# Kernel optimization log

Hardware: AMD Instinct MI355X
Metric: run time of the kernel (lower is better)

Reference implementation:

```python
import jax, jax.numpy as jnp
import numpy as np

B, S, D = 2, 2048, 768
E, F = 8, 3072  # num_experts, d_ff


def setup_inputs() -> dict:
    key = jax.random.key(0)
    k1, k2, k3, k4 = jax.random.split(key, 4)
    hidden_states = jax.random.normal(k1, (B, S, D), dtype=jnp.float32)
    w_router = jax.random.normal(k2, (D, E), dtype=jnp.float32) * (D ** -0.5)
    w1 = jax.random.normal(k3, (E, D, F), dtype=jnp.float32) * (D ** -0.5)
    w2 = jax.random.normal(k4, (E, F, D), dtype=jnp.float32) * (F ** -0.5)
    return {"hidden_states": hidden_states, "w_router": w_router, "w1": w1, "w2": w2}


def reference(hidden_states, w_router, w1, w2):
    # Router: top-1 (switch) routing.
    router_logits = jnp.einsum("bsd,de->bse", hidden_states, w_router)
    probs = jax.nn.softmax(router_logits, axis=-1)
    expert_index = jnp.argmax(probs, axis=-1)                      # [B,S] int
    router_mask = jax.nn.one_hot(expert_index, E, dtype=hidden_states.dtype)  # [B,S,E]
    router_probs = jnp.max(probs, axis=-1, keepdims=True)          # [B,S,1]

    # Expert FFN dispatch/combine (world_size=1 -> all_to_all is identity):
    # each token is processed by its assigned expert's relu-MLP.
    h1 = jax.nn.relu(jnp.einsum("bsd,edf->ebsf", hidden_states, w1))  # [E,B,S,F]
    h2 = jnp.einsum("ebsf,efd->ebsd", h1, w2)                          # [E,B,S,D]
    expert_out = jnp.einsum("ebsd,bse->bsd", h2, router_mask)          # combine

    out = router_probs * expert_out
    return out, router_logits, expert_index
```

## Files before the change

kernel.cpp:

```cpp
#include <hip/hip_runtime.h>
#include <hip/hip_bf16.h>

#define B_ 2
#define S_ 2048
#define D_ 768
#define E_ 8
#define F_ 3072
#define NT (B_*S_)
#define BM 128
#define MAXTILES 40

typedef __attribute__((ext_vector_type(8))) short bf16x8;
typedef __attribute__((ext_vector_type(4))) float f32x4;
typedef __attribute__((ext_vector_type(8))) unsigned short u16x8;

__device__ __forceinline__ unsigned short f2bf(float f){
  __hip_bfloat16 h = __float2bfloat16(f);
  return *reinterpret_cast<unsigned short*>(&h);
}

__device__ __forceinline__ void gll16(const void* g, void* l){
  __builtin_amdgcn_global_load_lds((const __attribute__((address_space(1))) unsigned int*)g,
                                   (__attribute__((address_space(3))) unsigned int*)l,
                                   16, 0, 0);
}

__global__ __launch_bounds__(256) void router_kernel(
    const float* __restrict__ x, const float* __restrict__ wr,
    float* __restrict__ logits_out, float* __restrict__ idx_out,
    float* __restrict__ probs, int* __restrict__ counts,
    int* __restrict__ bucket, unsigned short* __restrict__ xbf)
{
  const int wave = threadIdx.x >> 6, lane = threadIdx.x & 63;
  const int token = blockIdx.x * 4 + wave;
  const float* xp = x + (size_t)token * D_;

  float acc[E_] = {0.f,0.f,0.f,0.f,0.f,0.f,0.f,0.f};
  float xv[12];
  #pragma unroll
  for (int i = 0; i < 12; ++i){
    const int d = lane + i*64;
    const float v = xp[d];
    xv[i] = v;
    const float4 w0 = *(const float4*)(wr + d*8);
    const float4 w1 = *(const float4*)(wr + d*8 + 4);
    acc[0] += v*w0.x; acc[1] += v*w0.y; acc[2] += v*w0.z; acc[3] += v*w0.w;
    acc[4] += v*w1.x; acc[5] += v*w1.y; acc[6] += v*w1.z; acc[7] += v*w1.w;
  }
  #pragma unroll
  for (int j = 0; j < E_; ++j){
    float a = acc[j];
    for (int off = 32; off > 0; off >>= 1) a += __shfl_xor(a, off);
    acc[j] = a;
  }
  #pragma unroll
  for (int i = 0; i < 12; ++i){
    const int d = lane + i*64;
    xbf[(size_t)token * D_ + d] = f2bf(xv[i]);
  }
  if (lane == 0){
    float m = acc[0];
    #pragma unroll
    for (int j = 1; j < E_; ++j) m = fmaxf(m, acc[j]);
    float p[E_]; float s = 0.f;
    #pragma unroll
    for (int j = 0; j < E_; ++j){ p[j] = expf(acc[j] - m); s += p[j]; }
    const float inv = 1.0f / s;
    int best = 0; float bp = p[0]*inv;
    #pragma unroll
    for (int j = 1; j < E_; ++j){ const float pj = p[j]*inv; if (pj > bp){ bp = pj; best = j; } }
    float* lo = logits_out + (size_t)token * E_;
    #pragma unroll
    for (int j = 0; j < E_; ++j) lo[j] = acc[j];
    idx_out[token] = (float)best;
    probs[token] = bp;
    const int pos = atomicAdd(&counts[best], 1);
    bucket[best * NT + pos] = token;
  }
}

__global__ void build_tiles(const int* __restrict__ counts, int* __restrict__ meta)
{
  if (threadIdx.x == 0 && blockIdx.x == 0){
    int off = 0, n = 0;
    for (int e = 0; e < E_; ++e){
      const int c = counts[e];
      meta[1+e] = off;
      const int t = (c + BM - 1) / BM;
      for (int m = 0; m < t; ++m){ meta[16 + n] = (e << 16) | m; ++n; }
      off += c;
    }
    meta[0] = n;
  }
}

__global__ __launch_bounds__(256) void transpose_cvt(
    const float* __restrict__ in, unsigned short* __restrict__ outp, int R, int C)
{
  __shared__ float tile[64][65];
  const int e = blockIdx.z;
  const int r0 = blockIdx.y << 6, c0 = blockIdx.x << 6;
  const float* src = in + (size_t)e * R * C;
  unsigned short* dst = outp + (size_t)e * R * C;
  const int tid = threadIdx.x;
  {
    const int lr = tid >> 4, lc = (tid & 15) << 2;
    #pragma unroll
    for (int rr = 0; rr < 4; ++rr){
      const int row = (rr << 4) + lr;
      const float4 v = *(const float4*)(src + (size_t)(r0 + row) * C + c0 + lc);
      tile[row][lc+0] = v.x; tile[row][lc+1] = v.y;
      tile[row][lc+2] = v.z; tile[row][lc+3] = v.w;
    }
  }
  __syncthreads();
  {
    const int wrr = tid >> 3, wcc = (tid & 7) << 3;
    #pragma unroll
    for (int it = 0; it < 2; ++it){
      const int crow = (it << 5) + wrr;
      u16x8 o;
      #pragma unroll
      for (int j = 0; j < 8; ++j) o[j] = f2bf(tile[wcc + j][crow]);
      *(u16x8*)(dst + (size_t)(c0 + crow) * R + r0 + wcc) = o;
    }
  }
}

template<int K, int NCOLS, bool RELU>
__global__ __launch_bounds__(256) void gemm2ph(
    const unsigned short* __restrict__ Ab, const unsigned short* __restrict__ Bt,
    const int* __restrict__ counts, const int* __restrict__ bucket,
    const int* __restrict__ meta, const float* __restrict__ probs,
    unsigned short* __restrict__ h1out, float* __restrict__ fout)
{
  __shared__ unsigned short As[2][BM*64];
  __shared__ unsigned short Bs[2][128*64];
  if ((int)blockIdx.y >= meta[0]) return;
  const int em = meta[16 + blockIdx.y];
  const int e = em >> 16, mt = em & 0xffff;
  const int cnt = counts[e], off_e = meta[1+e];
  const int fbase = blockIdx.x << 7;
  const int tid = threadIdx.x, wave = tid >> 6, lane = tid & 63;
  const int* bkt = bucket + e * NT;
  const int rbase = mt * BM;

  const int rsub = lane >> 3;
  const int swzb = ((lane & 7) ^ rsub) << 4;
  const int cm1 = cnt - 1;
  const char* Asrc[4]; const char* Bsrc[4];
  #pragma unroll
  for (int c = 0; c < 4; ++c){
    const int cw = (c << 2) + wave;
    const int row = (cw << 3) + rsub;
    int gr = rbase + row; if (gr > cm1) gr = cm1;
    const size_t arow = RELU ? (size_t)bkt[gr] : (size_t)(off_e + gr);
    Asrc[c] = (const char*)(Ab + arow * K) + swzb;
    Bsrc[c] = (const char*)(Bt + ((size_t)e * NCOLS + fbase + row) * K) + swzb;
  }

  f32x4 acc[4][4] = {};
  const int wr = (wave >> 1) << 6;
  const int wc = (wave & 1) << 6;
  const int lo16 = lane & 15, hi = lane >> 4;
  constexpr int KT = K / 64;

  auto STAGE = [&](int buf, int kt){
    const int kb = kt << 7;
    #pragma unroll
    for (int c = 0; c < 4; ++c){
      const int cw = (c << 2) + wave;
      gll16(Asrc[c] + kb, (char*)&As[buf][0] + (cw << 10));
      gll16(Bsrc[c] + kb, (char*)&Bs[buf][0] + (cw << 10));
    }
  };
  auto COMPUTE = [&](int buf){
    const char* AsB = (const char*)&As[buf][0];
    const char* BsB = (const char*)&Bs[buf][0];
    #pragma unroll
    for (int kf = 0; kf < 2; ++kf){
      const int ko = (kf << 6) + (hi << 4);
      bf16x8 af[4], bv[4];
      #pragma unroll
      for (int mf = 0; mf < 4; ++mf){
        const int row = wr + (mf << 4) + lo16;
        af[mf] = *(const bf16x8*)(AsB + row * 128 + (ko ^ ((row & 7) << 4)));
      }
      #pragma unroll
      for (int nf = 0; nf < 4; ++nf){
        const int col = wc + (nf << 4) + lo16;
        bv[nf] = *(const bf16x8*)(BsB + col * 128 + (ko ^ ((col & 7) << 4)));
      }
      #pragma unroll
      for (int mf = 0; mf < 4; ++mf)
        #pragma unroll
        for (int nf = 0; nf < 4; ++nf)
          acc[mf][nf] = __builtin_amdgcn_mfma_f32_16x16x32_bf16(af[mf], bv[nf], acc[mf][nf], 0, 0, 0);
    }
  };

  STAGE(0, 0);
  __syncthreads();
  int cur = 0;
  for (int kt = 0; kt < KT - 1; ++kt){
    STAGE(cur ^ 1, kt + 1);
    COMPUTE(cur);
    __syncthreads();
    cur ^= 1;
  }
  COMPUTE(cur);

  const int rem = cnt - rbase;
  #pragma unroll
  for (int mf = 0; mf < 4; ++mf){
    #pragma unroll
    for (int j = 0; j < 4; ++j){
      const int r = wr + (mf << 4) + (hi << 2) + j;
      if (r < rem){
        if constexpr (RELU){
          const size_t crow = (size_t)(off_e + rbase + r);
          #pragma unroll
          for (int nf = 0; nf < 4; ++nf){
            float v = acc[mf][nf][j];
            v = v > 0.f ? v : 0.f;
            h1out[crow * NCOLS + fbase + wc + (nf << 4) + lo16] = f2bf(v);
          }
        } else {
          const int tok = bkt[rbase + r];
          const float p = probs[tok];
          #pragma unroll
          for (int nf = 0; nf < 4; ++nf)
            fout[(size_t)tok * NCOLS + fbase + wc + (nf << 4) + lo16] = p * acc[mf][nf][j];
        }
      }
    }
  }
}

extern "C" void kernel_launch(void* const* d_in, const int* in_sizes, int n_in,
                              void* d_out, int out_size, void* d_ws, size_t ws_size,
                              hipStream_t stream)
{
  const float* x  = (const float*)d_in[0];
  const float* wr = (const float*)d_in[1];
  const float* w1 = (const float*)d_in[2];
  const float* w2 = (const float*)d_in[3];
  float* out = (float*)d_out;

  constexpr size_t OUT_L = (size_t)NT * D_;
  constexpr size_t OUT_I = OUT_L + (size_t)NT * E_;

  char* ws = (char*)d_ws;
  int*            counts = (int*)ws;
  int*            meta   = (int*)(ws + 256);
  float*          probs  = (float*)(ws + 1024);
  int*            bucket = (int*)(ws + (32u << 10));
  unsigned short* xbf    = (unsigned short*)(ws + (256u << 10));
  unsigned short* w1t    = (unsigned short*)(ws + (8ull  << 20));
  unsigned short* w2t    = (unsigned short*)(ws + (48ull << 20));
  unsigned short* h1c    = (unsigned short*)(ws + (88ull << 20));

  hipMemsetAsync(counts, 0, E_ * sizeof(int), stream);

  router_kernel<<<dim3(NT/4), dim3(256), 0, stream>>>(
      x, wr, out + OUT_L, out + OUT_I, probs, counts, bucket, xbf);

  build_tiles<<<dim3(1), dim3(64), 0, stream>>>(counts, meta);

  transpose_cvt<<<dim3(F_/64, D_/64, E_), dim3(256), 0, stream>>>(w1, w1t, D_, F_);
  transpose_cvt<<<dim3(D_/64, F_/64, E_), dim3(256), 0, stream>>>(w2, w2t, F_, D_);

  gemm2ph<D_, F_, true><<<dim3(F_/128, MAXTILES), dim3(256), 0, stream>>>(
      xbf, w1t, counts, bucket, meta, nullptr, h1c, nullptr);

  gemm2ph<F_, D_, false><<<dim3(D_/128, MAXTILES), dim3(256), 0, stream>>>(
      h1c, w2t, counts, bucket, meta, probs, nullptr, out);
}
```

Measured before the change: 339.8 us.

## Gather tokens per expert, enlarge GEMM tiles, add split-K with atomic combine

The router now processes 16 tokens per wave and uses wave-ballot aggregated atomics to fill the per-expert buckets. A new gather_cvt kernel writes the tokens contiguously, grouped by expert, as bf16, so the first GEMM no longer does indirect row loads. Both expert GEMMs move to 256x128x128 tiles on 512-thread blocks, with an XCD-aware workgroup remap. The second GEMM is split in two along K and combines its halves with float atomicAdd into a zeroed output. In exchange, LDS double-buffering is dropped (load, sync, compute), and the change adds an extra memset, an extra kernel and atomic traffic.

New measurement: 362.5 us. 6.7% more time.

```diff
diff --git a/kernel.cpp b/kernel.cpp
--- a/kernel.cpp
+++ b/kernel.cpp
@@ -7,8 +7,10 @@
 #define E_ 8
 #define F_ 3072
 #define NT (B_*S_)
-#define BM 128
-#define MAXTILES 40
+#define BM 256
+#define BN 128
+#define BK 128
+#define MAXT 24
 
 typedef __attribute__((ext_vector_type(8))) short bf16x8;
 typedef __attribute__((ext_vector_type(4))) float f32x4;
@@ -28,54 +30,66 @@
 __global__ __launch_bounds__(256) void router_kernel(
     const float* __restrict__ x, const float* __restrict__ wr,
     float* __restrict__ logits_out, float* __restrict__ idx_out,
-    float* __restrict__ probs, int* __restrict__ counts,
-    int* __restrict__ bucket, unsigned short* __restrict__ xbf)
-{
+    float* __restrict__ probs, int* __restrict__ counts, int* __restrict__ bucket)
+{
+  __shared__ int sbest[64];
   const int wave = threadIdx.x >> 6, lane = threadIdx.x & 63;
-  const int token = blockIdx.x * 4 + wave;
-  const float* xp = x + (size_t)token * D_;
-
-  float acc[E_] = {0.f,0.f,0.f,0.f,0.f,0.f,0.f,0.f};
-  float xv[12];
-  #pragma unroll
-  for (int i = 0; i < 12; ++i){
-    const int d = lane + i*64;
-    const float v = xp[d];
-    xv[i] = v;
-    const float4 w0 = *(const float4*)(wr + d*8);
-    const float4 w1 = *(const float4*)(wr + d*8 + 4);
-    acc[0] += v*w0.x; acc[1] += v*w0.y; acc[2] += v*w0.z; acc[3] += v*w0.w;
-    acc[4] += v*w1.x; acc[5] += v*w1.y; acc[6] += v*w1.z; acc[7] += v*w1.w;
-  }
-  #pragma unroll
-  for (int j = 0; j < E_; ++j){
-    float a = acc[j];
-    for (int off = 32; off > 0; off >>= 1) a += __shfl_xor(a, off);
-    acc[j] = a;
-  }
-  #pragma unroll
-  for (int i = 0; i < 12; ++i){
-    const int d = lane + i*64;
-    xbf[(size_t)token * D_ + d] = f2bf(xv[i]);
-  }
-  if (lane == 0){
-    float m = acc[0];
-    #pragma unroll
-    for (int j = 1; j < E_; ++j) m = fmaxf(m, acc[j]);
-    float p[E_]; float s = 0.f;
-    #pragma unroll
-    for (int j = 0; j < E_; ++j){ p[j] = expf(acc[j] - m); s += p[j]; }
-    const float inv = 1.0f / s;
-    int best = 0; float bp = p[0]*inv;
-    #pragma unroll
-    for (int j = 1; j < E_; ++j){ const float pj = p[j]*inv; if (pj > bp){ bp = pj; best = j; } }
-    float* lo = logits_out + (size_t)token * E_;
-    #pragma unroll
-    for (int j = 0; j < E_; ++j) lo[j] = acc[j];
-    idx_out[token] = (float)best;
-    probs[token] = bp;
-    const int pos = atomicAdd(&counts[best], 1);
-    bucket[best * NT + pos] = token;
+  const int tbase = blockIdx.x * 64 + wave * 16;
+
+  for (int it = 0; it < 16; ++it){
+    const int token = tbase + it;
+    const float* xp = x + (size_t)token * D_;
+    float acc[E_] = {0.f,0.f,0.f,0.f,0.f,0.f,0.f,0.f};
+    #pragma unroll
+    for (int i = 0; i < 12; ++i){
+      const int d = lane + i*64;
+      const float v = xp[d];
+      const float4 w0 = *(const float4*)(wr + d*8);
+      const float4 w1v = *(const float4*)(wr + d*8 + 4);
+      acc[0] += v*w0.x; acc[1] += v*w0.y; acc[2] += v*w0.z; acc[3] += v*w0.w;
+      acc[4] += v*w1v.x; acc[5] += v*w1v.y; acc[6] += v*w1v.z; acc[7] += v*w1v.w;
+    }
+    #pragma unroll
+    for (int j = 0; j < E_; ++j){
+      float a = acc[j];
+      for (int off = 32; off > 0; off >>= 1) a += __shfl_xor(a, off);
+      acc[j] = a;
+    }
+    if (lane == 0){
+      float m = acc[0];
+      #pragma unroll
+      for (int j = 1; j < E_; ++j) m = fmaxf(m, acc[j]);
+      float p[E_]; float s = 0.f;
+      #pragma unroll
+      for (int j = 0; j < E_; ++j){ p[j] = expf(acc[j] - m); s += p[j]; }
+      const float inv = 1.0f / s;
+      int best = 0; float bp = p[0]*inv;
+      #pragma unroll
+      for (int j = 1; j < E_; ++j){ const float pj = p[j]*inv; if (pj > bp){ bp = pj; best = j; } }
+      float* lo = logits_out + (size_t)token * E_;
+      #pragma unroll
+      for (int j = 0; j < E_; ++j) lo[j] = acc[j];
+      idx_out[token] = (float)best;
+      probs[token] = bp;
+      sbest[wave*16 + it] = best;
+    }
+  }
+  __syncthreads();
+  if (threadIdx.x < 64){
+    const int l = threadIdx.x;
+    const int b = sbest[l];
+    unsigned long long m = 0;
+    #pragma unroll
+    for (int e2 = 0; e2 < E_; ++e2){
+      const unsigned long long me = __ballot(b == e2);
+      if (b == e2) m = me;
+    }
+    const int rank = __popcll(m & ((1ull << l) - 1ull));
+    const int leader = __ffsll((long long)m) - 1;
+    int baseval = 0;
+    if (l == leader) baseval = atomicAdd(&counts[b], __popcll(m));
+    baseval = __shfl(baseval, leader);
+    bucket[b * NT + baseval + rank] = blockIdx.x * 64 + l;
   }
 }
 
@@ -87,10 +101,31 @@
       const int c = counts[e];
       meta[1+e] = off;
       const int t = (c + BM - 1) / BM;
-      for (int m = 0; m < t; ++m){ meta[16 + n] = (e << 16) | m; ++n; }
+      for (int mtt = 0; mtt < t; ++mtt){ meta[16 + n] = (e << 16) | mtt; ++n; }
       off += c;
     }
     meta[0] = n;
+  }
+}
+
+__global__ __launch_bounds__(256) void gather_cvt(
+    const float* __restrict__ x, const int* __restrict__ bucket,
+    const int* __restrict__ meta, unsigned short* __restrict__ Ac)
+{
+  const int wave = threadIdx.x >> 6, lane = threadIdx.x & 63;
+  const int i = blockIdx.x * 4 + wave;
+  int e = 0;
+  #pragma unroll
+  for (int k = 1; k < E_; ++k) if (meta[1+k] <= i) e = k;
+  const int tok = bucket[e * NT + (i - meta[1+e])];
+  const float* src = x + (size_t)tok * D_;
+  unsigned short* dst = Ac + (size_t)i * D_;
+  #pragma unroll
+  for (int p = 0; p < 3; ++p){
+    const float4 v = *(const float4*)(src + p*256 + lane*4);
+    ushort4 o;
+    o.x = f2bf(v.x); o.y = f2bf(v.y); o.z = f2bf(v.z); o.w = f2bf(v.w);
+    *(ushort4*)(dst + p*256 + lane*4) = o;
   }
 }
 
@@ -127,69 +162,81 @@
   }
 }
 
-template<int K, int NCOLS, bool RELU>
-__global__ __launch_bounds__(256) void gemm2ph(
-    const unsigned short* __restrict__ Ab, const unsigned short* __restrict__ Bt,
+template<int KC, int KTOT, int NCOLS, bool RELU, int NSPLIT>
+__global__ __launch_bounds__(512) void gemm_g(
+    const unsigned short* __restrict__ Ac, const unsigned short* __restrict__ Bt,
     const int* __restrict__ counts, const int* __restrict__ bucket,
     const int* __restrict__ meta, const float* __restrict__ probs,
     unsigned short* __restrict__ h1out, float* __restrict__ fout)
 {
-  __shared__ unsigned short As[2][BM*64];
-  __shared__ unsigned short Bs[2][128*64];
-  if ((int)blockIdx.y >= meta[0]) return;
-  const int em = meta[16 + blockIdx.y];
+  __shared__ unsigned short As[BM*BK];
+  __shared__ unsigned short Bs[BN*BK];
+
+  const int nwg = gridDim.x * gridDim.y * gridDim.z;
+  const int orig = ((int)blockIdx.z * gridDim.y + blockIdx.y) * gridDim.x + blockIdx.x;
+  const int q = nwg >> 3, r = nwg & 7;
+  const int xcd = orig & 7, jj = orig >> 3;
+  const int wgid = (xcd < r ? xcd*(q+1) : r*(q+1) + (xcd - r)*q) + jj;
+  constexpr int NTC = NCOLS / BN;
+  const int nt = wgid % NTC;
+  const int rest = wgid / NTC;
+  const int ks = (NSPLIT > 1) ? (rest % NSPLIT) : 0;
+  const int tile = (NSPLIT > 1) ? (rest / NSPLIT) : rest;
+  if (tile >= meta[0]) return;
+
+  const int em = meta[16 + tile];
   const int e = em >> 16, mt = em & 0xffff;
   const int cnt = counts[e], off_e = meta[1+e];
-  const int fbase = blockIdx.x << 7;
+  const int rbase = mt * BM;
+  const int fbase = nt * BN;
   const int tid = threadIdx.x, wave = tid >> 6, lane = tid & 63;
-  const int* bkt = bucket + e * NT;
-  const int rbase = mt * BM;
-
-  const int rsub = lane >> 3;
-  const int swzb = ((lane & 7) ^ rsub) << 4;
+  const int rsub = lane >> 4;
+  const int c16 = lane & 15;
   const int cm1 = cnt - 1;
-  const char* Asrc[4]; const char* Bsrc[4];
+
+  const char* Asrc[8]; const char* Bsrc[4];
+  #pragma unroll
+  for (int c = 0; c < 8; ++c){
+    const int row = ((wave + (c << 3)) << 2) + rsub;
+    int gr = rbase + row; if (gr > cm1) gr = cm1;
+    Asrc[c] = (const char*)(Ac + (size_t)(off_e + gr) * KTOT + ks * KC)
+              + ((c16 ^ (row & 15)) << 4);
+  }
   #pragma unroll
   for (int c = 0; c < 4; ++c){
-    const int cw = (c << 2) + wave;
-    const int row = (cw << 3) + rsub;
-    int gr = rbase + row; if (gr > cm1) gr = cm1;
-    const size_t arow = RELU ? (size_t)bkt[gr] : (size_t)(off_e + gr);
-    Asrc[c] = (const char*)(Ab + arow * K) + swzb;
-    Bsrc[c] = (const char*)(Bt + ((size_t)e * NCOLS + fbase + row) * K) + swzb;
-  }
-
-  f32x4 acc[4][4] = {};
+    const int row = ((wave + (c << 3)) << 2) + rsub;
+    Bsrc[c] = (const char*)(Bt + ((size_t)e * NCOLS + fbase + row) * KTOT + ks * KC)
+              + ((c16 ^ (row & 15)) << 4);
+  }
+
   const int wr = (wave >> 1) << 6;
   const int wc = (wave & 1) << 6;
   const int lo16 = lane & 15, hi = lane >> 4;
-  constexpr int KT = K / 64;
-
-  auto STAGE = [&](int buf, int kt){
-    const int kb = kt << 7;
-    #pragma unroll
-    for (int c = 0; c < 4; ++c){
-      const int cw = (c << 2) + wave;
-      gll16(Asrc[c] + kb, (char*)&As[buf][0] + (cw << 10));
-      gll16(Bsrc[c] + kb, (char*)&Bs[buf][0] + (cw << 10));
-    }
-  };
-  auto COMPUTE = [&](int buf){
-    const char* AsB = (const char*)&As[buf][0];
-    const char* BsB = (const char*)&Bs[buf][0];
-    #pragma unroll
-    for (int kf = 0; kf < 2; ++kf){
+  f32x4 acc[4][4] = {};
+  constexpr int NKT = KC / BK;
+
+  for (int kt = 0; kt < NKT; ++kt){
+    const int kb = kt * (BK * 2);
+    #pragma unroll
+    for (int c = 0; c < 8; ++c)
+      gll16(Asrc[c] + kb, (char*)As + ((wave + (c << 3)) << 10));
+    #pragma unroll
+    for (int c = 0; c < 4; ++c)
+      gll16(Bsrc[c] + kb, (char*)Bs + ((wave + (c << 3)) << 10));
+    __syncthreads();
+    #pragma unroll
+    for (int kf = 0; kf < 4; ++kf){
       const int ko = (kf << 6) + (hi << 4);
       bf16x8 af[4], bv[4];
       #pragma unroll
       for (int mf = 0; mf < 4; ++mf){
         const int row = wr + (mf << 4) + lo16;
-        af[mf] = *(const bf16x8*)(AsB + row * 128 + (ko ^ ((row & 7) << 4)));
+        af[mf] = *(const bf16x8*)((const char*)As + row * 256 + (ko ^ ((row & 15) << 4)));
       }
       #pragma unroll
       for (int nf = 0; nf < 4; ++nf){
         const int col = wc + (nf << 4) + lo16;
-        bv[nf] = *(const bf16x8*)(BsB + col * 128 + (ko ^ ((col & 7) << 4)));
+        bv[nf] = *(const bf16x8*)((const char*)Bs + col * 256 + (ko ^ ((col & 15) << 4)));
       }
       #pragma unroll
       for (int mf = 0; mf < 4; ++mf)
@@ -197,28 +244,18 @@
         for (int nf = 0; nf < 4; ++nf)
           acc[mf][nf] = __builtin_amdgcn_mfma_f32_16x16x32_bf16(af[mf], bv[nf], acc[mf][nf], 0, 0, 0);
     }
-  };
-
-  STAGE(0, 0);
-  __syncthreads();
-  int cur = 0;
-  for (int kt = 0; kt < KT - 1; ++kt){
-    STAGE(cur ^ 1, kt + 1);
-    COMPUTE(cur);
     __syncthreads();
-    cur ^= 1;
-  }
-  COMPUTE(cur);
+  }
 
   const int rem = cnt - rbase;
   #pragma unroll
   for (int mf = 0; mf < 4; ++mf){
     #pragma unroll
     for (int j = 0; j < 4; ++j){
-      const int r = wr + (mf << 4) + (hi << 2) + j;
-      if (r < rem){
+      const int rr2 = wr + (mf << 4) + (hi << 2) + j;
+      if (rr2 < rem){
         if constexpr (RELU){
-          const size_t crow = (size_t)(off_e + rbase + r);
+          const size_t crow = (size_t)(off_e + rbase + rr2);
           #pragma unroll
           for (int nf = 0; nf < 4; ++nf){
             float v = acc[mf][nf][j];
@@ -226,11 +263,12 @@
             h1out[crow * NCOLS + fbase + wc + (nf << 4) + lo16] = f2bf(v);
           }
         } else {
-          const int tok = bkt[rbase + r];
+          const int tok = bucket[e * NT + rbase + rr2];
           const float p = probs[tok];
           #pragma unroll
           for (int nf = 0; nf < 4; ++nf)
-            fout[(size_t)tok * NCOLS + fbase + wc + (nf << 4) + lo16] = p * acc[mf][nf][j];
+            atomicAdd(&fout[(size_t)tok * NCOLS + fbase + wc + (nf << 4) + lo16],
+                      p * acc[mf][nf][j]);
         }
       }
     }
@@ -255,24 +293,27 @@
   int*            meta   = (int*)(ws + 256);
   float*          probs  = (float*)(ws + 1024);
   int*            bucket = (int*)(ws + (32u << 10));
-  unsigned short* xbf    = (unsigned short*)(ws + (256u << 10));
+  unsigned short* Ac     = (unsigned short*)(ws + (256u << 10));
   unsigned short* w1t    = (unsigned short*)(ws + (8ull  << 20));
   unsigned short* w2t    = (unsigned short*)(ws + (48ull << 20));
   unsigned short* h1c    = (unsigned short*)(ws + (88ull << 20));
 
   hipMemsetAsync(counts, 0, E_ * sizeof(int), stream);
-
-  router_kernel<<<dim3(NT/4), dim3(256), 0, stream>>>(
-      x, wr, out + OUT_L, out + OUT_I, probs, counts, bucket, xbf);
+  hipMemsetAsync(out, 0, OUT_L * sizeof(float), stream);
+
+  router_kernel<<<dim3(NT/64), dim3(256), 0, stream>>>(
+      x, wr, out + OUT_L, out + OUT_I, probs, counts, bucket);
 
   build_tiles<<<dim3(1), dim3(64), 0, stream>>>(counts, meta);
+
+  gather_cvt<<<dim3(NT/4), dim3(256), 0, stream>>>(x, bucket, meta, Ac);
 
   transpose_cvt<<<dim3(F_/64, D_/64, E_), dim3(256), 0, stream>>>(w1, w1t, D_, F_);
   transpose_cvt<<<dim3(D_/64, F_/64, E_), dim3(256), 0, stream>>>(w2, w2t, F_, D_);
 
-  gemm2ph<D_, F_, true><<<dim3(F_/128, MAXTILES), dim3(256), 0, stream>>>(
-      xbf, w1t, counts, bucket, meta, nullptr, h1c, nullptr);
-
-  gemm2ph<F_, D_, false><<<dim3(D_/128, MAXTILES), dim3(256), 0, stream>>>(
+  gemm_g<D_, D_, F_, true, 1><<<dim3(F_/BN, MAXT), dim3(512), 0, stream>>>(
+      Ac, w1t, counts, bucket, meta, nullptr, h1c, nullptr);
+
+  gemm_g<F_/2, F_, D_, false, 2><<<dim3(D_/BN, MAXT, 2), dim3(512), 0, stream>>>(
       h1c, w2t, counts, bucket, meta, probs, nullptr, out);
 }
```
